# Optimization experiments

Hardware: AMD Instinct MI355X
Metric: run time of the kernel (lower is better)

## Reference

```python
import jax, jax.numpy as jnp
import numpy as np


def setup_inputs() -> dict:
    key = jax.random.key(0)
    k1, k2 = jax.random.split(key)
    x = jax.random.normal(k1, (4096, 4), dtype=jnp.float32)
    support_vectors = jax.random.normal(k2, (4096, 4), dtype=jnp.float32)
    return {"x": x, "support_vectors": support_vectors}


def reference(x, support_vectors):
    # Quantum kernel: per (batch, support) pair, circuit is ry(x_k) then ry(-sv_k)
    # on each of 4 qubits starting from |0000>. Amplitude of |0000> is
    # prod_k cos((x_k - sv_k)/2); the module returns its absolute value.
    # x: [B, 4], support_vectors: [S, 4] -> out: [B, S]
    half_diff = (x[:, None, :] - support_vectors[None, :, :]) * 0.5  # [B, S, 4]
    return jnp.abs(jnp.prod(jnp.cos(half_diff), axis=-1))
```

## Files before the change

kernel.cpp:

```cpp
#include <hip/hip_runtime.h>
#include <hip/hip_bf16.h>


__global__ __launch_bounds__(256) void quantum_kernel(
    const float4* __restrict__ x,
    const float4* __restrict__ sv,
    float4* __restrict__ out,
    int s_quads)
{
    const int b  = blockIdx.y;
    const int q  = blockIdx.x * blockDim.x + threadIdx.x;
    if (q >= s_quads) return;

    const float4 xb = x[b];

    float4 r;
    float* rp = &r.x;
#pragma unroll
    for (int i = 0; i < 4; ++i) {
        const float4 s = sv[(size_t)4 * q + i];
        float p = __cosf((xb.x - s.x) * 0.5f)
                * __cosf((xb.y - s.y) * 0.5f)
                * __cosf((xb.z - s.z) * 0.5f)
                * __cosf((xb.w - s.w) * 0.5f);
        rp[i] = fabsf(p);
    }
    out[(size_t)b * s_quads + q] = r;
}

extern "C" void kernel_launch(void* const* d_in, const int* in_sizes, int n_in,
                              void* d_out, int out_size, void* d_ws, size_t ws_size,
                              hipStream_t stream) {
    const float4* x  = (const float4*)d_in[0];
    const float4* sv = (const float4*)d_in[1];
    float4* out = (float4*)d_out;

    const int B = in_sizes[0] / 4;
    const int S = in_sizes[1] / 4;
    const int s_quads = S / 4;

    const int block = 256;
    dim3 grid((s_quads + block - 1) / block, B);
    quantum_kernel<<<grid, block, 0, stream>>>(x, sv, out, s_quads);
}
```

Before: 87.48 us.

## Precompute half-angle sin/cos and use angle-difference identity instead of per-pair cosines

Adds a small pre-pass that computes sin and cos of the half-angles for every x row and support vector into the workspace. The main kernel then forms each cos((x-sv)/2) with one multiply and one FMA via the angle-difference identity, removing all transcendental calls from the B×S loop. This trades per-pair cosine evaluation for twice the support-vector load traffic (cached) and an extra kernel launch.

```diff
diff --git a/kernel.cpp b/kernel.cpp
--- a/kernel.cpp
+++ b/kernel.cpp
@@ -1,29 +1,50 @@
 #include <hip/hip_runtime.h>
 #include <hip/hip_bf16.h>
+#include <math.h>
 
 
-__global__ __launch_bounds__(256) void quantum_kernel(
+__global__ __launch_bounds__(256) void precompute_cs(
     const float4* __restrict__ x,
     const float4* __restrict__ sv,
+    float4* __restrict__ ws4,
+    int B, int total)
+{
+    int i = blockIdx.x * blockDim.x + threadIdx.x;
+    if (i >= total) return;
+    float4 v = (i < B) ? x[i] : sv[i - B];
+    float4 c, s;
+    sincosf(v.x * 0.5f, &s.x, &c.x);
+    sincosf(v.y * 0.5f, &s.y, &c.y);
+    sincosf(v.z * 0.5f, &s.z, &c.z);
+    sincosf(v.w * 0.5f, &s.w, &c.w);
+    ws4[2 * i]     = c;
+    ws4[2 * i + 1] = s;
+}
+
+__global__ __launch_bounds__(256) void quantum_kernel(
+    const float4* __restrict__ ws4,
     float4* __restrict__ out,
-    int s_quads)
+    int B, int s_quads)
 {
-    const int b  = blockIdx.y;
-    const int q  = blockIdx.x * blockDim.x + threadIdx.x;
+    const int b = blockIdx.y;
+    const int q = blockIdx.x * blockDim.x + threadIdx.x;
     if (q >= s_quads) return;
 
-    const float4 xb = x[b];
+    const float4 xc = ws4[2 * b];
+    const float4 xs = ws4[2 * b + 1];
 
     float4 r;
     float* rp = &r.x;
 #pragma unroll
     for (int i = 0; i < 4; ++i) {
-        const float4 s = sv[(size_t)4 * q + i];
-        float p = __cosf((xb.x - s.x) * 0.5f)
-                * __cosf((xb.y - s.y) * 0.5f)
-                * __cosf((xb.z - s.z) * 0.5f)
-                * __cosf((xb.w - s.w) * 0.5f);
-        rp[i] = fabsf(p);
+        const int sidx = 4 * q + i;
+        const float4 sc = ws4[2 * (B + sidx)];
+        const float4 ss = ws4[2 * (B + sidx) + 1];
+        float f0 = fmaf(xs.x, ss.x, xc.x * sc.x);
+        float f1 = fmaf(xs.y, ss.y, xc.y * sc.y);
+        float f2 = fmaf(xs.z, ss.z, xc.z * sc.z);
+        float f3 = fmaf(xs.w, ss.w, xc.w * sc.w);
+        rp[i] = fabsf((f0 * f1) * (f2 * f3));
     }
     out[(size_t)b * s_quads + q] = r;
 }
@@ -34,12 +55,16 @@
     const float4* x  = (const float4*)d_in[0];
     const float4* sv = (const float4*)d_in[1];
     float4* out = (float4*)d_out;
+    float4* ws4 = (float4*)d_ws;
 
     const int B = in_sizes[0] / 4;
     const int S = in_sizes[1] / 4;
+    const int total = B + S;
     const int s_quads = S / 4;
+
+    precompute_cs<<<(total + 255) / 256, 256, 0, stream>>>(x, sv, ws4, B, total);
 
     const int block = 256;
     dim3 grid((s_quads + block - 1) / block, B);
-    quantum_kernel<<<grid, block, 0, stream>>>(x, sv, out, s_quads);
+    quantum_kernel<<<grid, block, 0, stream>>>(ws4, out, B, s_quads);
 }
```

New measurement: 130.6 us. 49.3% more time.

## Expand cosine difference into precomputed cos/sin products with row blocking

Applied to the files above, without the earlier changes.

Uses the angle-difference identity so each output is a product of four FMA-combined cos/sin terms instead of four cosine evaluations. Row cos/sin are computed once per block into shared memory, and support-vector cos/sin are computed once per thread and reused across 16 batch rows. This removes most transcendental work, leaving the kernel bound by output writes. The launch now drops bounds checks and assumes dimensions divisible by the tile sizes.

```diff
diff --git a/kernel.cpp b/kernel.cpp
--- a/kernel.cpp
+++ b/kernel.cpp
@@ -1,37 +1,70 @@
 #include <hip/hip_runtime.h>
 #include <hip/hip_bf16.h>
+#include <math.h>
 
 
+#define BROWS 16
+
+__device__ __forceinline__ float qprod(const float4& xc, const float4& xs,
+                                       const float4& sc, const float4& ss) {
+    float f0 = fmaf(xs.x, ss.x, xc.x * sc.x);
+    float f1 = fmaf(xs.y, ss.y, xc.y * sc.y);
+    float f2 = fmaf(xs.z, ss.z, xc.z * sc.z);
+    float f3 = fmaf(xs.w, ss.w, xc.w * sc.w);
+    return fabsf((f0 * f1) * (f2 * f3));
+}
+
 __global__ __launch_bounds__(256) void quantum_kernel(
-    const float4* __restrict__ x,
+    const float*  __restrict__ x,
     const float4* __restrict__ sv,
     float4* __restrict__ out,
     int s_quads)
 {
-    const int b  = blockIdx.y;
-    const int q  = blockIdx.x * blockDim.x + threadIdx.x;
-    if (q >= s_quads) return;
+    __shared__ float xc_s[BROWS][4];
+    __shared__ float xs_s[BROWS][4];
 
-    const float4 xb = x[b];
+    const int tid = threadIdx.x;
+    const int q   = blockIdx.x * blockDim.x + tid;
+    const int b0  = blockIdx.y * BROWS;
 
-    float4 r;
-    float* rp = &r.x;
+    if (tid < BROWS * 4) {
+        const int row = tid >> 2, comp = tid & 3;
+        const float a = x[(size_t)(b0 + row) * 4 + comp] * 0.5f;
+        xc_s[row][comp] = __cosf(a);
+        xs_s[row][comp] = __sinf(a);
+    }
+
+    float4 sc[4], ss[4];
 #pragma unroll
-    for (int i = 0; i < 4; ++i) {
-        const float4 s = sv[(size_t)4 * q + i];
-        float p = __cosf((xb.x - s.x) * 0.5f)
-                * __cosf((xb.y - s.y) * 0.5f)
-                * __cosf((xb.z - s.z) * 0.5f)
-                * __cosf((xb.w - s.w) * 0.5f);
-        rp[i] = fabsf(p);
+    for (int j = 0; j < 4; ++j) {
+        const float4 v = sv[(size_t)4 * q + j];
+        sc[j].x = __cosf(v.x * 0.5f);  ss[j].x = __sinf(v.x * 0.5f);
+        sc[j].y = __cosf(v.y * 0.5f);  ss[j].y = __sinf(v.y * 0.5f);
+        sc[j].z = __cosf(v.z * 0.5f);  ss[j].z = __sinf(v.z * 0.5f);
+        sc[j].w = __cosf(v.w * 0.5f);  ss[j].w = __sinf(v.w * 0.5f);
     }
-    out[(size_t)b * s_quads + q] = r;
+
+    __syncthreads();
+
+    float4* orow = out + (size_t)b0 * s_quads + q;
+
+#pragma unroll 4
+    for (int i = 0; i < BROWS; ++i) {
+        float4 xc = { xc_s[i][0], xc_s[i][1], xc_s[i][2], xc_s[i][3] };
+        float4 xs = { xs_s[i][0], xs_s[i][1], xs_s[i][2], xs_s[i][3] };
+        float4 r;
+        r.x = qprod(xc, xs, sc[0], ss[0]);
+        r.y = qprod(xc, xs, sc[1], ss[1]);
+        r.z = qprod(xc, xs, sc[2], ss[2]);
+        r.w = qprod(xc, xs, sc[3], ss[3]);
+        orow[(size_t)i * s_quads] = r;
+    }
 }
 
 extern "C" void kernel_launch(void* const* d_in, const int* in_sizes, int n_in,
                               void* d_out, int out_size, void* d_ws, size_t ws_size,
                               hipStream_t stream) {
-    const float4* x  = (const float4*)d_in[0];
+    const float*  x  = (const float*)d_in[0];
     const float4* sv = (const float4*)d_in[1];
     float4* out = (float4*)d_out;
 
@@ -40,6 +73,6 @@
     const int s_quads = S / 4;
 
     const int block = 256;
-    dim3 grid((s_quads + block - 1) / block, B);
+    dim3 grid(s_quads / block, B / BROWS);
     quantum_kernel<<<grid, block, 0, stream>>>(x, sv, out, s_quads);
 }
```

After: 78.37 us. 1.12x faster.
